# Performance work log

Measured on AMD Instinct MI355X. Metric: run time of the kernel, lower is better.

The kernel has to match this reference:

```python
import jax, jax.numpy as jnp
import numpy as np


def _phase_idx(phase):
    t = 4.0 * phase
    i1 = jnp.mod(jnp.floor(t).astype(jnp.int32), 4)
    i0 = jnp.mod(i1 - 1, 4)
    i2 = jnp.mod(i1 + 1, 4)
    i3 = jnp.mod(i1 + 2, 4)
    w = jnp.mod(t, 1.0)  # fmod(t,1) for t>=0
    return w, i0, i1, i2, i3


def _cubic(a0, a1, a2, a3, w):
    # Catmull-Rom spline blend; a* have shape (B, ...), w broadcastable
    return (a1
            + w * (0.5 * a2 - 0.5 * a0)
            + w * w * (a0 - 2.5 * a1 + 2.0 * a2 - 0.5 * a3)
            + w * w * w * (1.5 * a1 - 1.5 * a2 + 0.5 * a3 - 0.5 * a0))


def setup_inputs() -> dict:
    key = jax.random.key(0)
    ks = jax.random.split(key, 8)
    B = 4096
    dims = [128, 256, 256, 128]

    def kaiming(k, shape):
        fan_in = shape[1]
        bound = np.sqrt(6.0 / fan_in)
        return jax.random.uniform(k, shape, jnp.float32, -bound, bound)

    inp = {
        "x": jax.random.normal(ks[0], (B, dims[0]), jnp.float32),
        "phase": jax.random.uniform(ks[1], (B,), jnp.float32),
    }
    for i in range(3):
        inp[f"w{i}"] = kaiming(ks[2 + i], (4, dims[i], dims[i + 1]))
        inp[f"b{i}"] = jnp.zeros((4, 1, dims[i + 1]), jnp.float32)
    return inp


def reference(x, phase, w0, b0, w1, b1, w2, b2):
    ws = [w0, w1, w2]
    bs = [b0, b1, b2]
    w, i0, i1, i2, i3 = _phase_idx(phase)
    w3 = w[:, None, None]  # (B,1,1) for weights and biases
    n = len(ws)
    for li in range(n):
        pw, pb = ws[li], bs[li]
        # per-sample interpolated weight (B, in, out) and bias (B, 1, out)
        weight = _cubic(pw[i0], pw[i1], pw[i2], pw[i3], w3)
        bias = _cubic(pb[i0], pb[i1], pb[i2], pb[i3], w3)
        x = jnp.einsum("bi,bio->bo", x, weight) + bias[:, 0, :]
        if li < n - 1:  # activation_at_last=False
            x = jax.nn.elu(x)
    return x
```

## Files before the change

kernel.cpp:

```cpp
#include <hip/hip_runtime.h>
#include <hip/hip_bf16.h>
#include <math.h>


typedef __attribute__((ext_vector_type(8))) short bf16x8;
typedef __attribute__((ext_vector_type(4))) float f32x4;

#define LDS_A0 0
#define LDS_A1 4096
#define LDS_A2 12288
#define LDS_CB 20480
#define LDS_B  21504
#define LDS_TOT (21504 + 131072)

#define VMW4()  asm volatile("s_waitcnt vmcnt(4)" ::: "memory")
#define VMW0()  asm volatile("s_waitcnt vmcnt(0)" ::: "memory")
#define LGKM0() asm volatile("s_waitcnt lgkmcnt(0)" ::: "memory")

static __device__ __forceinline__ void bar_keep_vmcnt() {
  asm volatile("s_waitcnt lgkmcnt(0)" ::: "memory");
  __builtin_amdgcn_s_barrier();
  asm volatile("" ::: "memory");
}

typedef const __attribute__((address_space(1))) unsigned char* gp1_t;
typedef __attribute__((address_space(3))) unsigned char* lp3_t;
static __device__ __forceinline__ void gl_lds16(const void* g, void* l) {
  __builtin_amdgcn_global_load_lds((gp1_t)g, (lp3_t)l, 16, 0, 0);
}

#define STAGE(sb, KIN, ci, slot) do {                                  \
    const unsigned short* _s = (sb) + (ci) * 32;                       \
    char* _d = myB + (slot) * 4096;                                    \
    gl_lds16(_s,             _d);                                      \
    gl_lds16(_s + (KIN),     _d + 1024);                               \
    gl_lds16(_s + 2 * (KIN), _d + 2048);                               \
    gl_lds16(_s + 3 * (KIN), _d + 3072);                               \
  } while (0)

static __device__ __forceinline__ unsigned short f2bf(float f) {
  union { float f; unsigned int u; } v; v.f = f;
  unsigned int r = v.u + 0x7fffu + ((v.u >> 16) & 1u);
  return (unsigned short)(r >> 16);
}

static __device__ __forceinline__ void catmull(float ph, float c[4]) {
  float t = 4.0f * ph;
  float ft = floorf(t);
  int i1 = ((int)ft) & 3;
  float w = t - ft;
  float w2 = w * w, w3 = w2 * w;
  float r0 = -0.5f * w + w2 - 0.5f * w3;
  float r1 = 1.0f - 2.5f * w2 + 1.5f * w3;
  float r2 = 0.5f * w + 2.0f * w2 - 1.5f * w3;
  float r3 = -0.5f * w2 + 0.5f * w3;
  c[(i1 + 3) & 3] = r0;
  c[i1]           = r1;
  c[(i1 + 1) & 3] = r2;
  c[(i1 + 2) & 3] = r3;
}

__global__ void k_wt_all(const float* __restrict__ w0, const float* __restrict__ w1,
                         const float* __restrict__ w2, unsigned short* __restrict__ t0,
                         unsigned short* __restrict__ t1, unsigned short* __restrict__ t2) {
  __shared__ float tile[32][33];
  int bid = blockIdx.x;
  const float* W; unsigned short* T; int R, C, idx;
  if (bid < 128)      { W = w0; T = t0; R = 512;  C = 256; idx = bid; }
  else if (bid < 384) { W = w1; T = t1; R = 1024; C = 256; idx = bid - 128; }
  else                { W = w2; T = t2; R = 1024; C = 128; idx = bid - 384; }
  int ntc = C >> 5;
  int tr = (idx / ntc) << 5;
  int tc = (idx % ntc) << 5;
  int tx = threadIdx.x, ty = threadIdx.y;
#pragma unroll
  for (int j = ty; j < 32; j += 8)
    tile[j][tx] = W[(size_t)(tr + j) * C + (tc + tx)];
  __syncthreads();
#pragma unroll
  for (int j = ty; j < 32; j += 8)
    T[(size_t)(tc + j) * R + (tr + tx)] = f2bf(tile[tx][j]);
}

static __device__ __forceinline__ void epi_mid(f32x4 a0, f32x4 a1, f32x4 a2, f32x4 a3,
                                               const float bv[4], const float* cbf,
                                               int colg, int quad, char* outBuf) {
  const int g = colg >> 3;
  const int j2 = (colg & 7) * 2;
#pragma unroll
  for (int r = 0; r < 4; ++r) {
    const int m = quad * 4 + r;
    const float4 c = *(const float4*)(cbf + m * 4);
    float y = c.x * (a0[r] + bv[0]) + c.y * (a1[r] + bv[1]) +
              c.z * (a2[r] + bv[2]) + c.w * (a3[r] + bv[3]);
    float a = y > 0.0f ? y : (__expf(y) - 1.0f);
    *(unsigned short*)(outBuf + m * 512 + (((g ^ (m & 15)) << 4) + j2)) = f2bf(a);
  }
}

#define MFMA4()                                                            \
  acc0 = __builtin_amdgcn_mfma_f32_16x16x32_bf16(av, bv0, acc0, 0, 0, 0);  \
  acc1 = __builtin_amdgcn_mfma_f32_16x16x32_bf16(av, bv1, acc1, 0, 0, 0);  \
  acc2 = __builtin_amdgcn_mfma_f32_16x16x32_bf16(av, bv2, acc2, 0, 0, 0);  \
  acc3 = __builtin_amdgcn_mfma_f32_16x16x32_bf16(av, bv3, acc3, 0, 0, 0)

#define LOADB()                                                \
  bf16x8 bv0 = *(const bf16x8*)(bs + bOff);                    \
  bf16x8 bv1 = *(const bf16x8*)(bs + 1024 + bOff);             \
  bf16x8 bv2 = *(const bf16x8*)(bs + 2048 + bOff);             \
  bf16x8 bv3 = *(const bf16x8*)(bs + 3072 + bOff)

__global__ __launch_bounds__(1024, 4) void k_fused(
    const float* __restrict__ x, const float* __restrict__ phase,
    const unsigned short* __restrict__ Wt0, const float* __restrict__ b0,
    const unsigned short* __restrict__ Wt1, const float* __restrict__ b1,
    const unsigned short* __restrict__ Wt2, const float* __restrict__ b2,
    float* __restrict__ out) {
  __shared__ __align__(1024) char smem[LDS_TOT];

  const int tid = threadIdx.x;
  const int lane = tid & 63;
  const int wid = tid >> 6;
  const int col = lane & 15;
  const int quad = lane >> 4;
  const int m0 = blockIdx.x * 16;
  const int colg = wid * 16 + col;
  const int cg = wid & 7, kh = wid >> 3;
  const int colg2 = cg * 16 + col;
  const int hi16 = (col & 12) << 4;
  const int lb = (quad ^ (col & 3)) << 4;
  const int bOff = col * 64 + quad * 16;

  char* myB = smem + LDS_B + wid * 8192;
  float* cbf = (float*)(smem + LDS_CB);

  const int colL = lane >> 2, qs = lane & 3;
  const unsigned short* sb0 = Wt0 + (size_t)(wid * 16 + colL) * 512 + qs * 8;
  const unsigned short* sb1 = Wt1 + (size_t)(wid * 16 + colL) * 1024 + qs * 8;
  const unsigned short* sb2 = Wt2 + (size_t)(cg * 16 + colL) * 1024 + kh * 128 + qs * 8;

  float4 xv = {0.f, 0.f, 0.f, 0.f};
  if (tid < 512)
    xv = *(const float4*)(x + (size_t)(m0 + (tid >> 5)) * 128 + (tid & 31) * 4);

  float bva[4], bvb[4], bvc[4];
#pragma unroll
  for (int k = 0; k < 4; ++k) {
    bva[k] = b0[k * 256 + colg];
    bvb[k] = b1[k * 256 + colg];
    bvc[k] = b2[k * 128 + colg2];
  }

  if (tid < 16) {
    float c[4];
    catmull(phase[m0 + tid], c);
    cbf[tid * 4 + 0] = c[0]; cbf[tid * 4 + 1] = c[1];
    cbf[tid * 4 + 2] = c[2]; cbf[tid * 4 + 3] = c[3];
  }

  STAGE(sb0, 128, 0, 0);
  STAGE(sb0, 128, 1, 1);

  if (tid < 512) {
    const int row = tid >> 5, seg = tid & 31;
    const int g = seg >> 1, h = seg & 1;
    short4 hv;
    hv.x = (short)f2bf(xv.x); hv.y = (short)f2bf(xv.y);
    hv.z = (short)f2bf(xv.z); hv.w = (short)f2bf(xv.w);
    *(short4*)(smem + LDS_A0 + row * 256 + ((g ^ (row & 15)) << 4) + h * 8) = hv;
  }
  bar_keep_vmcnt();

  f32x4 acc0, acc1, acc2, acc3;

  {
    acc0 = acc1 = acc2 = acc3 = (f32x4){0.f, 0.f, 0.f, 0.f};
    const char* aL = smem + LDS_A0 + col * 256 + lb;
#pragma unroll
    for (int i = 0; i < 4; ++i) {
      VMW4();
      const char* bs = myB + (i & 1) * 4096;
      bf16x8 av = *(const bf16x8*)(aL + ((i << 6) ^ hi16));
      LOADB();
      LGKM0();
      if (i == 0)      STAGE(sb0, 128, 2, 0);
      else if (i == 1) STAGE(sb0, 128, 3, 1);
      else if (i == 2) STAGE(sb1, 256, 0, 0);
      else             STAGE(sb1, 256, 1, 1);
      MFMA4();
    }
    epi_mid(acc0, acc1, acc2, acc3, bva, cbf, colg, quad, smem + LDS_A1);
  }
  bar_keep_vmcnt();

  {
    acc0 = acc1 = acc2 = acc3 = (f32x4){0.f, 0.f, 0.f, 0.f};
    const char* aL = smem + LDS_A1 + col * 512 + lb;
#pragma unroll
    for (int i = 0; i < 8; ++i) {
      VMW4();
      const char* bs = myB + (i & 1) * 4096;
      bf16x8 av = *(const bf16x8*)(aL + ((i << 6) ^ hi16));
      LOADB();
      LGKM0();
      if (i < 6)       STAGE(sb1, 256, i + 2, i & 1);
      else if (i == 6) STAGE(sb2, 256, 0, 0);
      else             STAGE(sb2, 256, 1, 1);
      MFMA4();
    }
    epi_mid(acc0, acc1, acc2, acc3, bvb, cbf, colg, quad, smem + LDS_A2);
  }
  bar_keep_vmcnt();

  {
    acc0 = acc1 = acc2 = acc3 = (f32x4){0.f, 0.f, 0.f, 0.f};
    const char* aL = smem + LDS_A2 + col * 512 + kh * 256 + lb;
#pragma unroll
    for (int i = 0; i < 4; ++i) {
      if (i < 3) { VMW4(); } else { VMW0(); }
      const char* bs = myB + (i & 1) * 4096;
      bf16x8 av = *(const bf16x8*)(aL + ((i << 6) ^ hi16));
      LOADB();
      if (i < 2) {
        LGKM0();
        if (i == 0) STAGE(sb2, 256, 2, 0);
        else        STAGE(sb2, 256, 3, 1);
      }
      MFMA4();
    }

    float part[4];
#pragma unroll
    for (int r = 0; r < 4; ++r) {
      const int m = quad * 4 + r;
      const float4 c = *(const float4*)(cbf + m * 4);
      part[r] = c.x * acc0[r] + c.y * acc1[r] + c.z * acc2[r] + c.w * acc3[r];
    }

    bar_keep_vmcnt();
    float* red = (float*)(smem + LDS_B);
    if (kh) {
#pragma unroll
      for (int r = 0; r < 4; ++r)
        red[cg * 272 + (quad * 4 + r) * 17 + col] = part[r];
    }
    bar_keep_vmcnt();
    if (!kh) {
#pragma unroll
      for (int r = 0; r < 4; ++r) {
        const int m = quad * 4 + r;
        const float4 c = *(const float4*)(cbf + m * 4);
        float y = part[r] + red[cg * 272 + m * 17 + col] +
                  c.x * bvc[0] + c.y * bvc[1] + c.z * bvc[2] + c.w * bvc[3];
        out[(size_t)(m0 + m) * 128 + colg2] = y;
      }
    }
  }
}

extern "C" void kernel_launch(void* const* d_in, const int* in_sizes, int n_in,
                              void* d_out, int out_size, void* d_ws, size_t ws_size,
                              hipStream_t stream) {
  const float* x     = (const float*)d_in[0];
  const float* phase = (const float*)d_in[1];
  const float* w0    = (const float*)d_in[2];
  const float* b0    = (const float*)d_in[3];
  const float* w1    = (const float*)d_in[4];
  const float* b1    = (const float*)d_in[5];
  const float* w2    = (const float*)d_in[6];
  const float* b2    = (const float*)d_in[7];
  float* out = (float*)d_out;

  char* ws = (char*)d_ws;
  unsigned short* Wt0 = (unsigned short*)ws;
  unsigned short* Wt1 = (unsigned short*)(ws + 262144);
  unsigned short* Wt2 = (unsigned short*)(ws + 262144 + 524288);

  k_wt_all<<<512, dim3(32, 8), 0, stream>>>(w0, w1, w2, Wt0, Wt1, Wt2);
  k_fused<<<256, 1024, 0, stream>>>(x, phase, Wt0, b0, Wt1, b1, Wt2, b2, out);
}
```

Baseline: 88.66 us.

## Keep spline coefficients in registers and restructure weight prefetch pipeline

Each lane now computes the Catmull-Rom coefficients for its own four rows in registers, instead of 16 threads writing them to LDS for everyone to read. The per-sample blended biases are also precomputed once per layer, which removes the repeated coefficient loads and per-element bias blending from the epilogues. The weight staging loop now issues the next chunk's global-to-LDS copy at the top of each iteration and drops the explicit lgkmcnt wait that stalled before each stage. In exchange, only one chunk is prefetched ahead instead of two, so less global load latency is hidden behind the MFMAs.

```diff
diff --git a/kernel.cpp b/kernel.cpp
--- a/kernel.cpp
+++ b/kernel.cpp
@@ -9,13 +9,11 @@
 #define LDS_A0 0
 #define LDS_A1 4096
 #define LDS_A2 12288
-#define LDS_CB 20480
-#define LDS_B  21504
-#define LDS_TOT (21504 + 131072)
+#define LDS_B  20480
+#define LDS_TOT (20480 + 131072)
 
 #define VMW4()  asm volatile("s_waitcnt vmcnt(4)" ::: "memory")
 #define VMW0()  asm volatile("s_waitcnt vmcnt(0)" ::: "memory")
-#define LGKM0() asm volatile("s_waitcnt lgkmcnt(0)" ::: "memory")
 
 static __device__ __forceinline__ void bar_keep_vmcnt() {
   asm volatile("s_waitcnt lgkmcnt(0)" ::: "memory");
@@ -83,16 +81,15 @@
 }
 
 static __device__ __forceinline__ void epi_mid(f32x4 a0, f32x4 a1, f32x4 a2, f32x4 a3,
-                                               const float bv[4], const float* cbf,
+                                               const float bm[4], const float cbr[4][4],
                                                int colg, int quad, char* outBuf) {
   const int g = colg >> 3;
   const int j2 = (colg & 7) * 2;
 #pragma unroll
   for (int r = 0; r < 4; ++r) {
     const int m = quad * 4 + r;
-    const float4 c = *(const float4*)(cbf + m * 4);
-    float y = c.x * (a0[r] + bv[0]) + c.y * (a1[r] + bv[1]) +
-              c.z * (a2[r] + bv[2]) + c.w * (a3[r] + bv[3]);
+    float y = cbr[r][0] * a0[r] + cbr[r][1] * a1[r] +
+              cbr[r][2] * a2[r] + cbr[r][3] * a3[r] + bm[r];
     float a = y > 0.0f ? y : (__expf(y) - 1.0f);
     *(unsigned short*)(outBuf + m * 512 + (((g ^ (m & 15)) << 4) + j2)) = f2bf(a);
   }
@@ -132,17 +129,12 @@
   const int bOff = col * 64 + quad * 16;
 
   char* myB = smem + LDS_B + wid * 8192;
-  float* cbf = (float*)(smem + LDS_CB);
 
   const int colL = lane >> 2, qs = lane & 3;
   const unsigned short* sb0 = Wt0 + (size_t)(wid * 16 + colL) * 512 + qs * 8;
   const unsigned short* sb1 = Wt1 + (size_t)(wid * 16 + colL) * 1024 + qs * 8;
   const unsigned short* sb2 = Wt2 + (size_t)(cg * 16 + colL) * 1024 + kh * 128 + qs * 8;
 
-  float4 xv = {0.f, 0.f, 0.f, 0.f};
-  if (tid < 512)
-    xv = *(const float4*)(x + (size_t)(m0 + (tid >> 5)) * 128 + (tid & 31) * 4);
-
   float bva[4], bvb[4], bvc[4];
 #pragma unroll
   for (int k = 0; k < 4; ++k) {
@@ -150,16 +142,26 @@
     bvb[k] = b1[k * 256 + colg];
     bvc[k] = b2[k * 128 + colg2];
   }
-
-  if (tid < 16) {
-    float c[4];
-    catmull(phase[m0 + tid], c);
-    cbf[tid * 4 + 0] = c[0]; cbf[tid * 4 + 1] = c[1];
-    cbf[tid * 4 + 2] = c[2]; cbf[tid * 4 + 3] = c[3];
-  }
+  float ph[4];
+#pragma unroll
+  for (int r = 0; r < 4; ++r) ph[r] = phase[m0 + quad * 4 + r];
+
+  float4 xv = {0.f, 0.f, 0.f, 0.f};
+  if (tid < 512)
+    xv = *(const float4*)(x + (size_t)(m0 + (tid >> 5)) * 128 + (tid & 31) * 4);
 
   STAGE(sb0, 128, 0, 0);
-  STAGE(sb0, 128, 1, 1);
+
+  float cbr[4][4];
+#pragma unroll
+  for (int r = 0; r < 4; ++r) catmull(ph[r], cbr[r]);
+  float bm0[4], bm1[4], bm2[4];
+#pragma unroll
+  for (int r = 0; r < 4; ++r) {
+    bm0[r] = cbr[r][0] * bva[0] + cbr[r][1] * bva[1] + cbr[r][2] * bva[2] + cbr[r][3] * bva[3];
+    bm1[r] = cbr[r][0] * bvb[0] + cbr[r][1] * bvb[1] + cbr[r][2] * bvb[2] + cbr[r][3] * bvb[3];
+    bm2[r] = cbr[r][0] * bvc[0] + cbr[r][1] * bvc[1] + cbr[r][2] * bvc[2] + cbr[r][3] * bvc[3];
+  }
 
   if (tid < 512) {
     const int row = tid >> 5, seg = tid & 31;
@@ -178,18 +180,15 @@
     const char* aL = smem + LDS_A0 + col * 256 + lb;
 #pragma unroll
     for (int i = 0; i < 4; ++i) {
+      if (i < 3) STAGE(sb0, 128, i + 1, (i + 1) & 1);
+      else       STAGE(sb1, 256, 0, 0);
       VMW4();
       const char* bs = myB + (i & 1) * 4096;
       bf16x8 av = *(const bf16x8*)(aL + ((i << 6) ^ hi16));
       LOADB();
-      LGKM0();
-      if (i == 0)      STAGE(sb0, 128, 2, 0);
-      else if (i == 1) STAGE(sb0, 128, 3, 1);
-      else if (i == 2) STAGE(sb1, 256, 0, 0);
-      else             STAGE(sb1, 256, 1, 1);
       MFMA4();
     }
-    epi_mid(acc0, acc1, acc2, acc3, bva, cbf, colg, quad, smem + LDS_A1);
+    epi_mid(acc0, acc1, acc2, acc3, bm0, cbr, colg, quad, smem + LDS_A1);
   }
   bar_keep_vmcnt();
 
@@ -198,17 +197,15 @@
     const char* aL = smem + LDS_A1 + col * 512 + lb;
 #pragma unroll
     for (int i = 0; i < 8; ++i) {
+      if (i < 7) STAGE(sb1, 256, i + 1, (i + 1) & 1);
+      else       STAGE(sb2, 256, 0, 0);
       VMW4();
       const char* bs = myB + (i & 1) * 4096;
       bf16x8 av = *(const bf16x8*)(aL + ((i << 6) ^ hi16));
       LOADB();
-      LGKM0();
-      if (i < 6)       STAGE(sb1, 256, i + 2, i & 1);
-      else if (i == 6) STAGE(sb2, 256, 0, 0);
-      else             STAGE(sb2, 256, 1, 1);
       MFMA4();
     }
-    epi_mid(acc0, acc1, acc2, acc3, bvb, cbf, colg, quad, smem + LDS_A2);
+    epi_mid(acc0, acc1, acc2, acc3, bm1, cbr, colg, quad, smem + LDS_A2);
   }
   bar_keep_vmcnt();
 
@@ -217,25 +214,19 @@
     const char* aL = smem + LDS_A2 + col * 512 + kh * 256 + lb;
 #pragma unroll
     for (int i = 0; i < 4; ++i) {
-      if (i < 3) { VMW4(); } else { VMW0(); }
+      if (i < 3) { STAGE(sb2, 256, i + 1, (i + 1) & 1); VMW4(); }
+      else       { VMW0(); }
       const char* bs = myB + (i & 1) * 4096;
       bf16x8 av = *(const bf16x8*)(aL + ((i << 6) ^ hi16));
       LOADB();
-      if (i < 2) {
-        LGKM0();
-        if (i == 0) STAGE(sb2, 256, 2, 0);
-        else        STAGE(sb2, 256, 3, 1);
-      }
       MFMA4();
     }
 
     float part[4];
 #pragma unroll
-    for (int r = 0; r < 4; ++r) {
-      const int m = quad * 4 + r;
-      const float4 c = *(const float4*)(cbf + m * 4);
-      part[r] = c.x * acc0[r] + c.y * acc1[r] + c.z * acc2[r] + c.w * acc3[r];
-    }
+    for (int r = 0; r < 4; ++r)
+      part[r] = cbr[r][0] * acc0[r] + cbr[r][1] * acc1[r] +
+                cbr[r][2] * acc2[r] + cbr[r][3] * acc3[r];
 
     bar_keep_vmcnt();
     float* red = (float*)(smem + LDS_B);
@@ -249,9 +240,7 @@
 #pragma unroll
       for (int r = 0; r < 4; ++r) {
         const int m = quad * 4 + r;
-        const float4 c = *(const float4*)(cbf + m * 4);
-        float y = part[r] + red[cg * 272 + m * 17 + col] +
-                  c.x * bvc[0] + c.y * bvc[1] + c.z * bvc[2] + c.w * bvc[3];
+        float y = part[r] + red[cg * 272 + m * 17 + col] + bm2[r];
         out[(size_t)(m0 + m) * 128 + colg2] = y;
       }
     }
```

New measurement: 90.77 us. 1.02x slower.

## Pre-pack weights into tile-contiguous bf16 blocks matching the MFMA fragment layout

Applied to the files above, without the earlier changes.

Replaces the transpose kernel with a packing kernel that writes each 16-column by 32-k chunk of every phase weight as contiguous 512-element blocks in the order the fused kernel stages them. Global-to-LDS copies then read fully contiguous 1 KB spans per wave instead of strided 64-byte pieces, and the LDS fragment offset becomes lane*16. This should improve load coalescing in the main kernel. The pack kernel does strided scalar reads of the fp32 weights, which may cost more than the old tiled transpose.

```diff
diff --git a/kernel.cpp b/kernel.cpp
--- a/kernel.cpp
+++ b/kernel.cpp
@@ -29,13 +29,13 @@
   __builtin_amdgcn_global_load_lds((gp1_t)g, (lp3_t)l, 16, 0, 0);
 }
 
-#define STAGE(sb, KIN, ci, slot) do {                                  \
-    const unsigned short* _s = (sb) + (ci) * 32;                       \
+#define STAGE(sb, ci, slot) do {                                       \
+    const unsigned short* _s = (sb) + (ci) * 2048;                     \
     char* _d = myB + (slot) * 4096;                                    \
-    gl_lds16(_s,             _d);                                      \
-    gl_lds16(_s + (KIN),     _d + 1024);                               \
-    gl_lds16(_s + 2 * (KIN), _d + 2048);                               \
-    gl_lds16(_s + 3 * (KIN), _d + 3072);                               \
+    gl_lds16(_s,        _d);                                           \
+    gl_lds16(_s +  512, _d + 1024);                                    \
+    gl_lds16(_s + 1024, _d + 2048);                                    \
+    gl_lds16(_s + 1536, _d + 3072);                                    \
   } while (0)
 
 static __device__ __forceinline__ unsigned short f2bf(float f) {
@@ -60,26 +60,35 @@
   c[(i1 + 2) & 3] = r3;
 }
 
-__global__ void k_wt_all(const float* __restrict__ w0, const float* __restrict__ w1,
-                         const float* __restrict__ w2, unsigned short* __restrict__ t0,
-                         unsigned short* __restrict__ t1, unsigned short* __restrict__ t2) {
-  __shared__ float tile[32][33];
-  int bid = blockIdx.x;
-  const float* W; unsigned short* T; int R, C, idx;
-  if (bid < 128)      { W = w0; T = t0; R = 512;  C = 256; idx = bid; }
-  else if (bid < 384) { W = w1; T = t1; R = 1024; C = 256; idx = bid - 128; }
-  else                { W = w2; T = t2; R = 1024; C = 128; idx = bid - 384; }
-  int ntc = C >> 5;
-  int tr = (idx / ntc) << 5;
-  int tc = (idx % ntc) << 5;
-  int tx = threadIdx.x, ty = threadIdx.y;
-#pragma unroll
-  for (int j = ty; j < 32; j += 8)
-    tile[j][tx] = W[(size_t)(tr + j) * C + (tc + tx)];
-  __syncthreads();
-#pragma unroll
-  for (int j = ty; j < 32; j += 8)
-    T[(size_t)(tc + j) * R + (tr + tx)] = f2bf(tile[tx][j]);
+__global__ __launch_bounds__(256) void k_pack(
+    const float* __restrict__ w0, const float* __restrict__ w1,
+    const float* __restrict__ w2, unsigned short* __restrict__ t0,
+    unsigned short* __restrict__ t1, unsigned short* __restrict__ t2) {
+  const int u = blockIdx.x;
+  const int t = threadIdx.x;
+  const int a = t >> 6, w = t & 63, col = w & 15, quad = w >> 4;
+  const float* W; unsigned short* T; size_t dst; int kr0, oc, Ostr;
+  if (u < 64) {
+    const int colgrp = u >> 2, ci = u & 3;
+    W = w0 + (size_t)a * 128 * 256; Ostr = 256;
+    kr0 = ci * 32 + quad * 8; oc = colgrp * 16 + col;
+    T = t0; dst = (size_t)colgrp * 8192 + ci * 2048 + a * 512 + w * 8;
+  } else if (u < 192) {
+    const int uu = u - 64, colgrp = uu >> 3, ci = uu & 7;
+    W = w1 + (size_t)a * 256 * 256; Ostr = 256;
+    kr0 = ci * 32 + quad * 8; oc = colgrp * 16 + col;
+    T = t1; dst = (size_t)colgrp * 16384 + ci * 2048 + a * 512 + w * 8;
+  } else {
+    const int uu = u - 192, cg = uu >> 3, kh = (uu >> 2) & 1, ci = uu & 3;
+    W = w2 + (size_t)a * 256 * 128; Ostr = 128;
+    kr0 = kh * 128 + ci * 32 + quad * 8; oc = cg * 16 + col;
+    T = t2; dst = (size_t)(cg * 2 + kh) * 8192 + ci * 2048 + a * 512 + w * 8;
+  }
+  bf16x8 v;
+#pragma unroll
+  for (int j = 0; j < 8; ++j)
+    v[j] = (short)f2bf(W[(size_t)(kr0 + j) * Ostr + oc]);
+  *(bf16x8*)(T + dst) = v;
 }
 
 static __device__ __forceinline__ void epi_mid(f32x4 a0, f32x4 a1, f32x4 a2, f32x4 a3,
@@ -129,15 +138,14 @@
   const int colg2 = cg * 16 + col;
   const int hi16 = (col & 12) << 4;
   const int lb = (quad ^ (col & 3)) << 4;
-  const int bOff = col * 64 + quad * 16;
+  const int bOff = lane * 16;
 
   char* myB = smem + LDS_B + wid * 8192;
   float* cbf = (float*)(smem + LDS_CB);
 
-  const int colL = lane >> 2, qs = lane & 3;
-  const unsigned short* sb0 = Wt0 + (size_t)(wid * 16 + colL) * 512 + qs * 8;
-  const unsigned short* sb1 = Wt1 + (size_t)(wid * 16 + colL) * 1024 + qs * 8;
-  const unsigned short* sb2 = Wt2 + (size_t)(cg * 16 + colL) * 1024 + kh * 128 + qs * 8;
+  const unsigned short* sb0 = Wt0 + (size_t)wid * 8192 + lane * 8;
+  const unsigned short* sb1 = Wt1 + (size_t)wid * 16384 + lane * 8;
+  const unsigned short* sb2 = Wt2 + (size_t)(cg * 2 + kh) * 8192 + lane * 8;
 
   float4 xv = {0.f, 0.f, 0.f, 0.f};
   if (tid < 512)
@@ -158,8 +166,8 @@
     cbf[tid * 4 + 2] = c[2]; cbf[tid * 4 + 3] = c[3];
   }
 
-  STAGE(sb0, 128, 0, 0);
-  STAGE(sb0, 128, 1, 1);
+  STAGE(sb0, 0, 0);
+  STAGE(sb0, 1, 1);
 
   if (tid < 512) {
     const int row = tid >> 5, seg = tid & 31;
@@ -183,10 +191,10 @@
       bf16x8 av = *(const bf16x8*)(aL + ((i << 6) ^ hi16));
       LOADB();
       LGKM0();
-      if (i == 0)      STAGE(sb0, 128, 2, 0);
-      else if (i == 1) STAGE(sb0, 128, 3, 1);
-      else if (i == 2) STAGE(sb1, 256, 0, 0);
-      else             STAGE(sb1, 256, 1, 1);
+      if (i == 0)      STAGE(sb0, 2, 0);
+      else if (i == 1) STAGE(sb0, 3, 1);
+      else if (i == 2) STAGE(sb1, 0, 0);
+      else             STAGE(sb1, 1, 1);
       MFMA4();
     }
     epi_mid(acc0, acc1, acc2, acc3, bva, cbf, colg, quad, smem + LDS_A1);
@@ -203,9 +211,9 @@
       bf16x8 av = *(const bf16x8*)(aL + ((i << 6) ^ hi16));
       LOADB();
       LGKM0();
-      if (i < 6)       STAGE(sb1, 256, i + 2, i & 1);
-      else if (i == 6) STAGE(sb2, 256, 0, 0);
-      else             STAGE(sb2, 256, 1, 1);
+      if (i < 6)       STAGE(sb1, i + 2, i & 1);
+      else if (i == 6) STAGE(sb2, 0, 0);
+      else             STAGE(sb2, 1, 1);
       MFMA4();
     }
     epi_mid(acc0, acc1, acc2, acc3, bvb, cbf, colg, quad, smem + LDS_A2);
@@ -223,8 +231,8 @@
       LOADB();
       if (i < 2) {
         LGKM0();
-        if (i == 0) STAGE(sb2, 256, 2, 0);
-        else        STAGE(sb2, 256, 3, 1);
+        if (i == 0) STAGE(sb2, 2, 0);
+        else        STAGE(sb2, 3, 1);
       }
       MFMA4();
     }
@@ -276,6 +284,6 @@
   unsigned short* Wt1 = (unsigned short*)(ws + 262144);
   unsigned short* Wt2 = (unsigned short*)(ws + 262144 + 524288);
 
-  k_wt_all<<<512, dim3(32, 8), 0, stream>>>(w0, w1, w2, Wt0, Wt1, Wt2);
+  k_pack<<<256, 256, 0, stream>>>(w0, w1, w2, Wt0, Wt1, Wt2);
   k_fused<<<256, 1024, 0, stream>>>(x, phase, Wt0, b0, Wt1, b1, Wt2, b2, out);
 }
```

New measurement: 83.94 us. -5.3%, faster.
